# Kernel optimization log

Hardware: AMD Instinct MI355X
Metric: run time of the kernel (lower is better)

## Reference

```python
import jax, jax.numpy as jnp
import numpy as np

N_NODES = 100000
D = 40


def sgconv(x, src, dst, W, b, n_nodes):
    """PyG SGConv with K=1: symmetric gcn_norm with self-loops, then linear."""
    # add self loops
    loop = jnp.arange(n_nodes, dtype=src.dtype)
    s = jnp.concatenate([src, loop])
    d = jnp.concatenate([dst, loop])
    ones = jnp.ones(s.shape[0], dtype=x.dtype)
    deg = jax.ops.segment_sum(ones, d, num_segments=n_nodes)
    dinv = jnp.where(deg > 0, jax.lax.rsqrt(deg), 0.0)
    norm = dinv[s] * dinv[d]                      # [E+N]
    msg = norm[:, None] * x[s]                    # gather + scale, [E+N, D]
    agg = jax.ops.segment_sum(msg, d, num_segments=n_nodes)  # scatter-add, [N, D]
    return agg @ W.T + b


def setup_inputs() -> dict:
    key = jax.random.key(0)
    k1, k2, k3, k4, k5, k6 = jax.random.split(key, 6)
    x = jax.random.normal(k1, (N_NODES, D), dtype=jnp.float32)
    edge_index = jax.random.randint(k2, (2, 1600000), 0, N_NODES, dtype=jnp.int64)
    s = 1.0 / np.sqrt(D)
    W1 = jax.random.uniform(k3, (D, D), jnp.float32, -s, s)
    b1 = jax.random.uniform(k4, (D,), jnp.float32, -s, s)
    W2 = jax.random.uniform(k5, (D, D), jnp.float32, -s, s)
    b2 = jax.random.uniform(k6, (D,), jnp.float32, -s, s)
    return {"x": x, "edge_index": edge_index, "W1": W1, "b1": b1, "W2": W2, "b2": b2}


def reference(x, edge_index, W1, b1, W2, b2):
    src, dst = edge_index[0], edge_index[1]
    n = x.shape[0]
    h = jax.nn.relu(sgconv(x, src, dst, W1, b1, n))
    out = sgconv(h, src, dst, W2, b2, n)
    return out.reshape(n * out.shape[1])  # generalizes x.view(1600)
```

## Files before the change

kernel.cpp:

```cpp
#include <hip/hip_runtime.h>
#include <hip/hip_fp16.h>

#define DD 40
#define PITER 32
#define NP 512
#define SROW_LD 44
#define SWT_LD 41
#define GC_PAD 16

__global__ void k_binA(const int* __restrict__ src, const int* __restrict__ dst,
                       int* __restrict__ gcur, unsigned* __restrict__ ebin,
                       int E, int PS, unsigned M, int CAPB) {
  __shared__ int hist[NP];
  __shared__ int curs[NP];
  const int tid = threadIdx.x;
  hist[tid] = 0;
  hist[tid + 256] = 0;
  __syncthreads();
  const int base = blockIdx.x * (256 * PITER);
  for (int it = 0; it < PITER; ++it) {
    int i = base + it * 256 + tid;
    if (i < E) {
      unsigned t = (unsigned)dst[i];
      int b = (int)(((unsigned long long)t * M) >> 31);
      atomicAdd(&hist[b], 1);
    }
  }
  __syncthreads();
#pragma unroll
  for (int q = 0; q < 2; ++q) {
    int b = tid + q * 256;
    int h = hist[b];
    int old = h ? atomicAdd(&gcur[b * GC_PAD], h) : 0;
    curs[b] = b * CAPB + old;
  }
  __syncthreads();
  for (int it = 0; it < PITER; ++it) {
    int i = base + it * 256 + tid;
    if (i < E) {
      unsigned t = (unsigned)dst[i];
      int b = (int)(((unsigned long long)t * M) >> 31);
      unsigned local = t - (unsigned)(b * PS);
      int pos = atomicAdd(&curs[b], 1);
      ebin[pos] = (local << 17) | (unsigned)src[i];
    }
  }
}

__global__ __launch_bounds__(256) void k_partB(
    const unsigned* __restrict__ ebin, const int* __restrict__ gcur,
    int* __restrict__ ideg, int* __restrict__ cursor, float* __restrict__ dinv,
    int* __restrict__ es, int PS, int CAPB, int CAPE, int n) {
  __shared__ int sdeg[256];
  __shared__ int sbuf[2][256];
  __shared__ int scur[256];
  const int p = blockIdx.x;
  const int tid = threadIdx.x;
  const int start = p * CAPB;
  const int cnt = gcur[p * GC_PAD];

  sdeg[tid] = 0;
  __syncthreads();
  for (int i = tid; i < cnt; i += 256) atomicAdd(&sdeg[ebin[start + i] >> 17], 1);
  __syncthreads();

  int v = sdeg[tid];
  sbuf[0][tid] = v;
  __syncthreads();
  int pi = 0;
  for (int off = 1; off < 256; off <<= 1) {
    int x = sbuf[pi][tid];
    if (tid >= off) x += sbuf[pi][tid - off];
    sbuf[pi ^ 1][tid] = x;
    __syncthreads();
    pi ^= 1;
  }
  int incl = sbuf[pi][tid];
  scur[tid] = incl - v;

  const int node = p * PS + tid;
  if (tid < PS && node < n) {
    ideg[node] = v;
    cursor[node] = p * CAPE + incl;
    dinv[node] = rsqrtf((float)(v + 1));
  }
  __syncthreads();

  for (int i = tid; i < cnt; i += 256) {
    unsigned pk = ebin[start + i];
    int l = (int)(pk >> 17);
    int pos = atomicAdd(&scur[l], 1);
    es[p * CAPE + pos] = (int)(pk & 0x1FFFFu);
  }
}

__global__ void k_prescale(const float4* __restrict__ x4, const float* __restrict__ dinv,
                           uint2* __restrict__ xs8, int n4) {
  int i = blockIdx.x * blockDim.x + threadIdx.x;
  if (i < n4) {
    float w = dinv[i / 10];
    float4 v = x4[i];
    __half2 ha = __float22half2_rn(make_float2(v.x * w, v.y * w));
    __half2 hb = __float22half2_rn(make_float2(v.z * w, v.w * w));
    uint2 u;
    u.x = *(unsigned*)&ha;
    u.y = *(unsigned*)&hb;
    xs8[i] = u;
  }
}

template <int OUT_HALF>
__global__ __launch_bounds__(256) void k_layer(
    const uint4* __restrict__ in4, const int* __restrict__ es,
    const int* __restrict__ ideg, const int* __restrict__ cursor,
    const float* __restrict__ dinv, const float* __restrict__ W,
    const float* __restrict__ bias, float* __restrict__ outf,
    __half2* __restrict__ outh, int n) {
  __shared__ float sWT[DD * SWT_LD];
  __shared__ float sb[DD];
  __shared__ float srow[48][SROW_LD];
  const int tid = threadIdx.x;

  const int w = tid >> 6, lane = tid & 63;
  const int g = lane / 5, pos = lane - g * 5;
  const int v = blockIdx.x * 48 + w * 12 + g;

#define ACC8(U, A)                                   \
  {                                                  \
    const __half2* hh = (const __half2*)&(U);        \
    float2 f0 = __half22float2(hh[0]);               \
    float2 f1 = __half22float2(hh[1]);               \
    float2 f2 = __half22float2(hh[2]);               \
    float2 f3 = __half22float2(hh[3]);               \
    A[0] += f0.x; A[1] += f0.y; A[2] += f1.x;        \
    A[3] += f1.y; A[4] += f2.x; A[5] += f2.y;        \
    A[6] += f3.x; A[7] += f3.y;                      \
  }

  if (g < 12 && v < n) {
    const int e1 = cursor[v];
    int e = e1 - ideg[v];
    float a[8], b[8];
    {
      uint4 u = in4[(size_t)v * 5 + pos];
      const __half2* hh = (const __half2*)&u;
      float2 f0 = __half22float2(hh[0]);
      float2 f1 = __half22float2(hh[1]);
      float2 f2 = __half22float2(hh[2]);
      float2 f3 = __half22float2(hh[3]);
      a[0] = f0.x; a[1] = f0.y; a[2] = f1.x; a[3] = f1.y;
      a[4] = f2.x; a[5] = f2.y; a[6] = f3.x; a[7] = f3.y;
#pragma unroll
      for (int q = 0; q < 8; ++q) b[q] = 0.f;
    }
    int n0, n1, n2, n3, n4, n5, n6, n7;
    bool have = (e + 7 < e1);
    if (have) {
      n0 = es[e];     n1 = es[e + 1]; n2 = es[e + 2]; n3 = es[e + 3];
      n4 = es[e + 4]; n5 = es[e + 5]; n6 = es[e + 6]; n7 = es[e + 7];
    }
    while (have) {
      int s0 = n0, s1 = n1, s2 = n2, s3 = n3, s4 = n4, s5 = n5, s6 = n6, s7 = n7;
      int en = e + 8;
      have = (en + 7 < e1);
      if (have) {
        n0 = es[en];     n1 = es[en + 1]; n2 = es[en + 2]; n3 = es[en + 3];
        n4 = es[en + 4]; n5 = es[en + 5]; n6 = es[en + 6]; n7 = es[en + 7];
      }
      uint4 u0 = in4[(size_t)s0 * 5 + pos];
      uint4 u1 = in4[(size_t)s1 * 5 + pos];
      uint4 u2 = in4[(size_t)s2 * 5 + pos];
      uint4 u3 = in4[(size_t)s3 * 5 + pos];
      uint4 u4 = in4[(size_t)s4 * 5 + pos];
      uint4 u5 = in4[(size_t)s5 * 5 + pos];
      uint4 u6 = in4[(size_t)s6 * 5 + pos];
      uint4 u7 = in4[(size_t)s7 * 5 + pos];
      ACC8(u0, a); ACC8(u1, b); ACC8(u2, a); ACC8(u3, b);
      ACC8(u4, a); ACC8(u5, b); ACC8(u6, a); ACC8(u7, b);
      e = en;
    }
    for (; e + 3 < e1; e += 4) {
      int s0 = es[e], s1 = es[e + 1], s2 = es[e + 2], s3 = es[e + 3];
      uint4 u0 = in4[(size_t)s0 * 5 + pos];
      uint4 u1 = in4[(size_t)s1 * 5 + pos];
      uint4 u2 = in4[(size_t)s2 * 5 + pos];
      uint4 u3 = in4[(size_t)s3 * 5 + pos];
      ACC8(u0, a); ACC8(u1, b); ACC8(u2, a); ACC8(u3, b);
    }
    for (; e < e1; ++e) {
      uint4 uu = in4[(size_t)es[e] * 5 + pos];
      ACC8(uu, a);
    }
    float* r = &srow[w * 12 + g][pos * 8];
#pragma unroll
    for (int q = 0; q < 8; ++q) r[q] = a[q] + b[q];
  }

  for (int t = tid; t < DD * DD; t += 256) sWT[(t % DD) * SWT_LD + t / DD] = W[t];
  if (tid < DD) sb[tid] = bias[tid];
  __syncthreads();

  if (OUT_HALF) {
    for (int i = tid; i < 48 * 20; i += 256) {
      int l = i / 20, jj = i - l * 20;
      int vv = blockIdx.x * 48 + l;
      if (vv < n) {
        float dv = dinv[vv];
        const float* row = srow[l];
        float s0 = 0.f, s1 = 0.f;
#pragma unroll
        for (int k = 0; k < DD; ++k) {
          s0 = fmaf(row[k], sWT[k * SWT_LD + 2 * jj], s0);
          s1 = fmaf(row[k], sWT[k * SWT_LD + 2 * jj + 1], s1);
        }
        s0 = fmaf(s0, dv, sb[2 * jj]);
        s1 = fmaf(s1, dv, sb[2 * jj + 1]);
        s0 = fmaxf(s0, 0.f) * dv;
        s1 = fmaxf(s1, 0.f) * dv;
        outh[(size_t)vv * 20 + jj] = __float22half2_rn(make_float2(s0, s1));
      }
    }
  } else {
    for (int i = tid; i < 48 * DD; i += 256) {
      int l = i / DD, j = i - l * DD;
      int vv = blockIdx.x * 48 + l;
      if (vv < n) {
        float dv = dinv[vv];
        const float* row = srow[l];
        float acc = 0.f;
#pragma unroll
        for (int k = 0; k < DD; ++k) acc = fmaf(row[k], sWT[k * SWT_LD + j], acc);
        outf[(size_t)vv * DD + j] = fmaf(acc, dv, sb[j]);
      }
    }
  }
#undef ACC8
}

extern "C" void kernel_launch(void* const* d_in, const int* in_sizes, int n_in,
                              void* d_out, int out_size, void* d_ws, size_t ws_size,
                              hipStream_t stream) {
  const float* x = (const float*)d_in[0];
  const int* ei = (const int*)d_in[1];
  const float* W1 = (const float*)d_in[2];
  const float* b1 = (const float*)d_in[3];
  const float* W2 = (const float*)d_in[4];
  const float* b2 = (const float*)d_in[5];

  const int n = in_sizes[0] / DD;
  const int E = in_sizes[1] / 2;
  const int* src = ei;
  const int* dst = ei + E;
  const int n4 = n * (DD / 4);
  const int PS = (n + NP - 1) / NP;
  const unsigned M = (unsigned)((((unsigned long long)1 << 31) + PS - 1) / PS);
  const int CAPB = E / NP + 512;
  const int CAPE = CAPB;
  const int NCH = (E + 256 * PITER - 1) / (256 * PITER);

  float* out = (float*)d_out;

  char* w = (char*)d_ws;
  float* dinv = (float*)w;   w += (size_t)n * 4;
  int* ideg = (int*)w;       w += (size_t)n * 4;
  int* cursor = (int*)w;     w += (size_t)n * 4;
  int* gcur = (int*)w;       w += (size_t)NP * GC_PAD * 4;
  char* ebin_hs = w;         w += (size_t)n * DD * 2;
  int* es = (int*)w;         w += (size_t)NP * CAPE * 4;
  uint2* xs8 = (uint2*)w;    w += (size_t)n * DD * 2;

  unsigned* ebin = (unsigned*)ebin_hs;
  uint2* hs8 = (uint2*)ebin_hs;

  hipMemsetAsync(gcur, 0, (size_t)NP * GC_PAD * 4, stream);

  k_binA<<<NCH, 256, 0, stream>>>(src, dst, gcur, ebin, E, PS, M, CAPB);
  k_partB<<<NP, 256, 0, stream>>>(ebin, gcur, ideg, cursor, dinv, es, PS, CAPB, CAPE, n);
  k_prescale<<<(n4 + 255) / 256, 256, 0, stream>>>((const float4*)x, dinv, xs8, n4);

  const int NBK = (n + 47) / 48;
  k_layer<1><<<NBK, 256, 0, stream>>>((const uint4*)xs8, es, ideg, cursor, dinv,
                                      W1, b1, nullptr, (__half2*)hs8, n);
  k_layer<0><<<NBK, 256, 0, stream>>>((const uint4*)hs8, es, ideg, cursor, dinv,
                                      W2, b2, out, nullptr, n);
}
```

Baseline: 153.4 us.

## Split neighbor lists by source half and sort edges locally before binning

k_binA now sorts each chunk's edges by destination bin in shared memory before writing them out. This turns scattered global stores into more contiguous runs. Each edge is also tagged by whether its source lies in the lower or upper half of the node range. k_partB orders each node's neighbor list as low-half sources first, then high-half sources, and records the split point. k_layer gathers the low half, hits a block barrier, then gathers the high half, aiming for better cache locality on the feature gathers. The costs are extra shared memory, lower occupancy in k_binA, a barrier that can stall warps, and an extra per-node array.

```diff
diff --git a/kernel.cpp b/kernel.cpp
--- a/kernel.cpp
+++ b/kernel.cpp
@@ -7,65 +7,37 @@
 #define SROW_LD 44
 #define SWT_LD 41
 #define GC_PAD 16
-
-__global__ void k_binA(const int* __restrict__ src, const int* __restrict__ dst,
-                       int* __restrict__ gcur, unsigned* __restrict__ ebin,
-                       int E, int PS, unsigned M, int CAPB) {
+#define BAE (256 * PITER)
+
+__global__ __launch_bounds__(256) void k_binA(
+    const int* __restrict__ src, const int* __restrict__ dst,
+    int* __restrict__ gcur, unsigned* __restrict__ ebin,
+    int E, int PS, unsigned M, int CAPB, int H) {
+  __shared__ unsigned ssort[BAE];
+  __shared__ int sdest[BAE];
   __shared__ int hist[NP];
+  __shared__ int binstart[NP];
   __shared__ int curs[NP];
+  __shared__ int win[NP];
+  __shared__ int sbuf[2][256];
   const int tid = threadIdx.x;
+  const int base = blockIdx.x * BAE;
+  const int cnt = min(BAE, E - base);
+
   hist[tid] = 0;
   hist[tid + 256] = 0;
   __syncthreads();
-  const int base = blockIdx.x * (256 * PITER);
   for (int it = 0; it < PITER; ++it) {
-    int i = base + it * 256 + tid;
-    if (i < E) {
-      unsigned t = (unsigned)dst[i];
+    int i = it * 256 + tid;
+    if (i < cnt) {
+      unsigned t = (unsigned)dst[base + i];
       int b = (int)(((unsigned long long)t * M) >> 31);
       atomicAdd(&hist[b], 1);
     }
   }
   __syncthreads();
-#pragma unroll
-  for (int q = 0; q < 2; ++q) {
-    int b = tid + q * 256;
-    int h = hist[b];
-    int old = h ? atomicAdd(&gcur[b * GC_PAD], h) : 0;
-    curs[b] = b * CAPB + old;
-  }
-  __syncthreads();
-  for (int it = 0; it < PITER; ++it) {
-    int i = base + it * 256 + tid;
-    if (i < E) {
-      unsigned t = (unsigned)dst[i];
-      int b = (int)(((unsigned long long)t * M) >> 31);
-      unsigned local = t - (unsigned)(b * PS);
-      int pos = atomicAdd(&curs[b], 1);
-      ebin[pos] = (local << 17) | (unsigned)src[i];
-    }
-  }
-}
-
-__global__ __launch_bounds__(256) void k_partB(
-    const unsigned* __restrict__ ebin, const int* __restrict__ gcur,
-    int* __restrict__ ideg, int* __restrict__ cursor, float* __restrict__ dinv,
-    int* __restrict__ es, int PS, int CAPB, int CAPE, int n) {
-  __shared__ int sdeg[256];
-  __shared__ int sbuf[2][256];
-  __shared__ int scur[256];
-  const int p = blockIdx.x;
-  const int tid = threadIdx.x;
-  const int start = p * CAPB;
-  const int cnt = gcur[p * GC_PAD];
-
-  sdeg[tid] = 0;
-  __syncthreads();
-  for (int i = tid; i < cnt; i += 256) atomicAdd(&sdeg[ebin[start + i] >> 17], 1);
-  __syncthreads();
-
-  int v = sdeg[tid];
-  sbuf[0][tid] = v;
+  int h0 = hist[2 * tid], h1 = hist[2 * tid + 1];
+  sbuf[0][tid] = h0 + h1;
   __syncthreads();
   int pi = 0;
   for (int off = 1; off < 256; off <<= 1) {
@@ -75,12 +47,80 @@
     __syncthreads();
     pi ^= 1;
   }
+  int excl = sbuf[pi][tid] - (h0 + h1);
+  binstart[2 * tid] = excl;
+  binstart[2 * tid + 1] = excl + h0;
+  curs[2 * tid] = excl;
+  curs[2 * tid + 1] = excl + h0;
+#pragma unroll
+  for (int q = 0; q < 2; ++q) {
+    int b = 2 * tid + q;
+    int h = hist[b];
+    win[b] = h ? (b * CAPB + atomicAdd(&gcur[b * GC_PAD], h)) : 0;
+  }
+  __syncthreads();
+  for (int it = 0; it < PITER; ++it) {
+    int i = it * 256 + tid;
+    if (i < cnt) {
+      unsigned t = (unsigned)dst[base + i];
+      int b = (int)(((unsigned long long)t * M) >> 31);
+      unsigned local = t - (unsigned)(b * PS);
+      unsigned s = (unsigned)src[base + i];
+      unsigned hf = (s >= (unsigned)H) ? 0x80000000u : 0u;
+      int pos = atomicAdd(&curs[b], 1);
+      ssort[pos] = hf | (local << 17) | s;
+      sdest[pos] = win[b] + (pos - binstart[b]);
+    }
+  }
+  __syncthreads();
+  for (int k = tid; k < cnt; k += 256) ebin[sdest[k]] = ssort[k];
+}
+
+__global__ __launch_bounds__(256) void k_partB(
+    const unsigned* __restrict__ ebin, const int* __restrict__ gcur,
+    int* __restrict__ ideg, int* __restrict__ dlo, int* __restrict__ cursor,
+    float* __restrict__ dinv, int* __restrict__ es,
+    int PS, int CAPB, int CAPE, int n) {
+  __shared__ int slo[256], shi[256];
+  __shared__ int sbuf[2][256];
+  __shared__ int clo[256], chi[256];
+  const int p = blockIdx.x;
+  const int tid = threadIdx.x;
+  const int start = p * CAPB;
+  const int cnt = gcur[p * GC_PAD];
+
+  slo[tid] = 0;
+  shi[tid] = 0;
+  __syncthreads();
+  for (int i = tid; i < cnt; i += 256) {
+    unsigned pk = ebin[start + i];
+    int l = (int)((pk >> 17) & 0xFF);
+    if (pk & 0x80000000u) atomicAdd(&shi[l], 1);
+    else atomicAdd(&slo[l], 1);
+  }
+  __syncthreads();
+
+  int vlo = slo[tid], vhi = shi[tid];
+  int v = vlo + vhi;
+  sbuf[0][tid] = v;
+  __syncthreads();
+  int pi = 0;
+  for (int off = 1; off < 256; off <<= 1) {
+    int x = sbuf[pi][tid];
+    if (tid >= off) x += sbuf[pi][tid - off];
+    sbuf[pi ^ 1][tid] = x;
+    __syncthreads();
+    pi ^= 1;
+  }
   int incl = sbuf[pi][tid];
-  scur[tid] = incl - v;
+  int rstart = incl - v;
+  clo[tid] = rstart;
+  chi[tid] = rstart + vlo;
 
   const int node = p * PS + tid;
   if (tid < PS && node < n) {
     ideg[node] = v;
+    dlo[node] = vlo;
     cursor[node] = p * CAPE + incl;
     dinv[node] = rsqrtf((float)(v + 1));
   }
@@ -88,8 +128,8 @@
 
   for (int i = tid; i < cnt; i += 256) {
     unsigned pk = ebin[start + i];
-    int l = (int)(pk >> 17);
-    int pos = atomicAdd(&scur[l], 1);
+    int l = (int)((pk >> 17) & 0xFF);
+    int pos = (pk & 0x80000000u) ? atomicAdd(&chi[l], 1) : atomicAdd(&clo[l], 1);
     es[p * CAPE + pos] = (int)(pk & 0x1FFFFu);
   }
 }
@@ -112,10 +152,10 @@
 template <int OUT_HALF>
 __global__ __launch_bounds__(256) void k_layer(
     const uint4* __restrict__ in4, const int* __restrict__ es,
-    const int* __restrict__ ideg, const int* __restrict__ cursor,
-    const float* __restrict__ dinv, const float* __restrict__ W,
-    const float* __restrict__ bias, float* __restrict__ outf,
-    __half2* __restrict__ outh, int n) {
+    const int* __restrict__ ideg, const int* __restrict__ dlo,
+    const int* __restrict__ cursor, const float* __restrict__ dinv,
+    const float* __restrict__ W, const float* __restrict__ bias,
+    float* __restrict__ outf, __half2* __restrict__ outh, int n) {
   __shared__ float sWT[DD * SWT_LD];
   __shared__ float sb[DD];
   __shared__ float srow[48][SROW_LD];
@@ -124,6 +164,7 @@
   const int w = tid >> 6, lane = tid & 63;
   const int g = lane / 5, pos = lane - g * 5;
   const int v = blockIdx.x * 48 + w * 12 + g;
+  const bool act = (g < 12 && v < n);
 
 #define ACC8(U, A)                                   \
   {                                                  \
@@ -137,24 +178,27 @@
     A[6] += f3.x; A[7] += f3.y;                      \
   }
 
-  if (g < 12 && v < n) {
-    const int e1 = cursor[v];
-    int e = e1 - ideg[v];
-    float a[8], b[8];
-    {
-      uint4 u = in4[(size_t)v * 5 + pos];
-      const __half2* hh = (const __half2*)&u;
-      float2 f0 = __half22float2(hh[0]);
-      float2 f1 = __half22float2(hh[1]);
-      float2 f2 = __half22float2(hh[2]);
-      float2 f3 = __half22float2(hh[3]);
-      a[0] = f0.x; a[1] = f0.y; a[2] = f1.x; a[3] = f1.y;
-      a[4] = f2.x; a[5] = f2.y; a[6] = f3.x; a[7] = f3.y;
-#pragma unroll
-      for (int q = 0; q < 8; ++q) b[q] = 0.f;
-    }
+  float a[8], b[8];
+  int mid = 0, e1 = 0;
+  if (act) {
+    e1 = cursor[v];
+    int e0 = e1 - ideg[v];
+    mid = e0 + dlo[v];
+    uint4 u = in4[(size_t)v * 5 + pos];
+    const __half2* hh = (const __half2*)&u;
+    float2 f0 = __half22float2(hh[0]);
+    float2 f1 = __half22float2(hh[1]);
+    float2 f2 = __half22float2(hh[2]);
+    float2 f3 = __half22float2(hh[3]);
+    a[0] = f0.x; a[1] = f0.y; a[2] = f1.x; a[3] = f1.y;
+    a[4] = f2.x; a[5] = f2.y; a[6] = f3.x; a[7] = f3.y;
+#pragma unroll
+    for (int q = 0; q < 8; ++q) b[q] = 0.f;
+  }
+
+  auto gather = [&](int e, int eend) {
     int n0, n1, n2, n3, n4, n5, n6, n7;
-    bool have = (e + 7 < e1);
+    bool have = (e + 7 < eend);
     if (have) {
       n0 = es[e];     n1 = es[e + 1]; n2 = es[e + 2]; n3 = es[e + 3];
       n4 = es[e + 4]; n5 = es[e + 5]; n6 = es[e + 6]; n7 = es[e + 7];
@@ -162,7 +206,7 @@
     while (have) {
       int s0 = n0, s1 = n1, s2 = n2, s3 = n3, s4 = n4, s5 = n5, s6 = n6, s7 = n7;
       int en = e + 8;
-      have = (en + 7 < e1);
+      have = (en + 7 < eend);
       if (have) {
         n0 = es[en];     n1 = es[en + 1]; n2 = es[en + 2]; n3 = es[en + 3];
         n4 = es[en + 4]; n5 = es[en + 5]; n6 = es[en + 6]; n7 = es[en + 7];
@@ -179,7 +223,7 @@
       ACC8(u4, a); ACC8(u5, b); ACC8(u6, a); ACC8(u7, b);
       e = en;
     }
-    for (; e + 3 < e1; e += 4) {
+    for (; e + 3 < eend; e += 4) {
       int s0 = es[e], s1 = es[e + 1], s2 = es[e + 2], s3 = es[e + 3];
       uint4 u0 = in4[(size_t)s0 * 5 + pos];
       uint4 u1 = in4[(size_t)s1 * 5 + pos];
@@ -187,10 +231,16 @@
       uint4 u3 = in4[(size_t)s3 * 5 + pos];
       ACC8(u0, a); ACC8(u1, b); ACC8(u2, a); ACC8(u3, b);
     }
-    for (; e < e1; ++e) {
+    for (; e < eend; ++e) {
       uint4 uu = in4[(size_t)es[e] * 5 + pos];
       ACC8(uu, a);
     }
+  };
+
+  if (act) gather(e1 - ideg[v] + 0, mid);
+  __syncthreads();
+  if (act) {
+    gather(mid, e1);
     float* r = &srow[w * 12 + g][pos * 8];
 #pragma unroll
     for (int q = 0; q < 8; ++q) r[q] = a[q] + b[q];
@@ -256,13 +306,15 @@
   const unsigned M = (unsigned)((((unsigned long long)1 << 31) + PS - 1) / PS);
   const int CAPB = E / NP + 512;
   const int CAPE = CAPB;
-  const int NCH = (E + 256 * PITER - 1) / (256 * PITER);
+  const int NCH = (E + BAE - 1) / BAE;
+  const int H = n / 2;
 
   float* out = (float*)d_out;
 
   char* w = (char*)d_ws;
   float* dinv = (float*)w;   w += (size_t)n * 4;
   int* ideg = (int*)w;       w += (size_t)n * 4;
+  int* dloA = (int*)w;       w += (size_t)n * 4;
   int* cursor = (int*)w;     w += (size_t)n * 4;
   int* gcur = (int*)w;       w += (size_t)NP * GC_PAD * 4;
   char* ebin_hs = w;         w += (size_t)n * DD * 2;
@@ -274,13 +326,14 @@
 
   hipMemsetAsync(gcur, 0, (size_t)NP * GC_PAD * 4, stream);
 
-  k_binA<<<NCH, 256, 0, stream>>>(src, dst, gcur, ebin, E, PS, M, CAPB);
-  k_partB<<<NP, 256, 0, stream>>>(ebin, gcur, ideg, cursor, dinv, es, PS, CAPB, CAPE, n);
+  k_binA<<<NCH, 256, 0, stream>>>(src, dst, gcur, ebin, E, PS, M, CAPB, H);
+  k_partB<<<NP, 256, 0, stream>>>(ebin, gcur, ideg, dloA, cursor, dinv, es,
+                                  PS, CAPB, CAPE, n);
   k_prescale<<<(n4 + 255) / 256, 256, 0, stream>>>((const float4*)x, dinv, xs8, n4);
 
   const int NBK = (n + 47) / 48;
-  k_layer<1><<<NBK, 256, 0, stream>>>((const uint4*)xs8, es, ideg, cursor, dinv,
+  k_layer<1><<<NBK, 256, 0, stream>>>((const uint4*)xs8, es, ideg, dloA, cursor, dinv,
                                       W1, b1, nullptr, (__half2*)hs8, n);
-  k_layer<0><<<NBK, 256, 0, stream>>>((const uint4*)hs8, es, ideg, cursor, dinv,
+  k_layer<0><<<NBK, 256, 0, stream>>>((const uint4*)hs8, es, ideg, dloA, cursor, dinv,
                                       W2, b2, out, nullptr, n);
 }
```

After: 155.4 us. No clear change (+1.3%).

## Sort edge bins in LDS before scatter and split node features into aligned arrays

Applied to the files above, without the earlier changes.

The binning kernel now counting-sorts each chunk of edges by bin in shared memory, then writes them out contiguously, so global writes to ebin are coalesced runs instead of scattered atomics-driven stores. Node features (fp16, 80 bytes) are split into a 64-byte main array plus a 16-byte tail array, so the four main gather lanes read from 64-byte-aligned rows with shift addressing rather than a multiply by 5. The cost is extra shared memory in binA (about 64KB), which lowers occupancy, plus an added scan. The partB index gets masked to 8 bits.

```diff
diff --git a/kernel.cpp b/kernel.cpp
--- a/kernel.cpp
+++ b/kernel.cpp
@@ -7,44 +7,71 @@
 #define SROW_LD 44
 #define SWT_LD 41
 #define GC_PAD 16
-
-__global__ void k_binA(const int* __restrict__ src, const int* __restrict__ dst,
-                       int* __restrict__ gcur, unsigned* __restrict__ ebin,
-                       int E, int PS, unsigned M, int CAPB) {
+#define BAE (256 * PITER)
+
+__global__ __launch_bounds__(256) void k_binA(
+    const int* __restrict__ src, const int* __restrict__ dst,
+    int* __restrict__ gcur, unsigned* __restrict__ ebin,
+    int E, int PS, unsigned M, int CAPB) {
+  __shared__ unsigned ssort[BAE];
+  __shared__ int sdest[BAE];
   __shared__ int hist[NP];
+  __shared__ int binstart[NP];
   __shared__ int curs[NP];
+  __shared__ int win[NP];
+  __shared__ int sbuf[2][256];
   const int tid = threadIdx.x;
+  const int base = blockIdx.x * BAE;
+  const int cnt = min(BAE, E - base);
+
   hist[tid] = 0;
   hist[tid + 256] = 0;
   __syncthreads();
-  const int base = blockIdx.x * (256 * PITER);
   for (int it = 0; it < PITER; ++it) {
-    int i = base + it * 256 + tid;
-    if (i < E) {
-      unsigned t = (unsigned)dst[i];
+    int i = it * 256 + tid;
+    if (i < cnt) {
+      unsigned t = (unsigned)dst[base + i];
       int b = (int)(((unsigned long long)t * M) >> 31);
       atomicAdd(&hist[b], 1);
     }
   }
   __syncthreads();
+  int h0 = hist[2 * tid], h1 = hist[2 * tid + 1];
+  sbuf[0][tid] = h0 + h1;
+  __syncthreads();
+  int pi = 0;
+  for (int off = 1; off < 256; off <<= 1) {
+    int x = sbuf[pi][tid];
+    if (tid >= off) x += sbuf[pi][tid - off];
+    sbuf[pi ^ 1][tid] = x;
+    __syncthreads();
+    pi ^= 1;
+  }
+  int excl = sbuf[pi][tid] - (h0 + h1);
+  binstart[2 * tid] = excl;
+  binstart[2 * tid + 1] = excl + h0;
+  curs[2 * tid] = excl;
+  curs[2 * tid + 1] = excl + h0;
 #pragma unroll
   for (int q = 0; q < 2; ++q) {
-    int b = tid + q * 256;
+    int b = 2 * tid + q;
     int h = hist[b];
-    int old = h ? atomicAdd(&gcur[b * GC_PAD], h) : 0;
-    curs[b] = b * CAPB + old;
+    win[b] = h ? (b * CAPB + atomicAdd(&gcur[b * GC_PAD], h)) : 0;
   }
   __syncthreads();
   for (int it = 0; it < PITER; ++it) {
-    int i = base + it * 256 + tid;
-    if (i < E) {
-      unsigned t = (unsigned)dst[i];
+    int i = it * 256 + tid;
+    if (i < cnt) {
+      unsigned t = (unsigned)dst[base + i];
       int b = (int)(((unsigned long long)t * M) >> 31);
       unsigned local = t - (unsigned)(b * PS);
       int pos = atomicAdd(&curs[b], 1);
-      ebin[pos] = (local << 17) | (unsigned)src[i];
-    }
-  }
+      ssort[pos] = (local << 17) | (unsigned)src[base + i];
+      sdest[pos] = win[b] + (pos - binstart[b]);
+    }
+  }
+  __syncthreads();
+  for (int k = tid; k < cnt; k += 256) ebin[sdest[k]] = ssort[k];
 }
 
 __global__ __launch_bounds__(256) void k_partB(
@@ -61,7 +88,8 @@
 
   sdeg[tid] = 0;
   __syncthreads();
-  for (int i = tid; i < cnt; i += 256) atomicAdd(&sdeg[ebin[start + i] >> 17], 1);
+  for (int i = tid; i < cnt; i += 256)
+    atomicAdd(&sdeg[(ebin[start + i] >> 17) & 0xFF], 1);
   __syncthreads();
 
   int v = sdeg[tid];
@@ -88,34 +116,40 @@
 
   for (int i = tid; i < cnt; i += 256) {
     unsigned pk = ebin[start + i];
-    int l = (int)(pk >> 17);
+    int l = (int)((pk >> 17) & 0xFF);
     int pos = atomicAdd(&scur[l], 1);
     es[p * CAPE + pos] = (int)(pk & 0x1FFFFu);
   }
 }
 
 __global__ void k_prescale(const float4* __restrict__ x4, const float* __restrict__ dinv,
-                           uint2* __restrict__ xs8, int n4) {
+                           uint4* __restrict__ xs_m, uint4* __restrict__ xs_t, int n5) {
   int i = blockIdx.x * blockDim.x + threadIdx.x;
-  if (i < n4) {
-    float w = dinv[i / 10];
-    float4 v = x4[i];
-    __half2 ha = __float22half2_rn(make_float2(v.x * w, v.y * w));
-    __half2 hb = __float22half2_rn(make_float2(v.z * w, v.w * w));
-    uint2 u;
-    u.x = *(unsigned*)&ha;
-    u.y = *(unsigned*)&hb;
-    xs8[i] = u;
+  if (i < n5) {
+    int node = i / 5, part = i - node * 5;
+    float w = dinv[node];
+    float4 va = x4[node * 10 + part * 2];
+    float4 vb = x4[node * 10 + part * 2 + 1];
+    __half2 h0 = __float22half2_rn(make_float2(va.x * w, va.y * w));
+    __half2 h1 = __float22half2_rn(make_float2(va.z * w, va.w * w));
+    __half2 h2 = __float22half2_rn(make_float2(vb.x * w, vb.y * w));
+    __half2 h3 = __float22half2_rn(make_float2(vb.z * w, vb.w * w));
+    uint4 u;
+    u.x = *(unsigned*)&h0; u.y = *(unsigned*)&h1;
+    u.z = *(unsigned*)&h2; u.w = *(unsigned*)&h3;
+    if (part < 4) xs_m[(size_t)node * 4 + part] = u;
+    else xs_t[node] = u;
   }
 }
 
 template <int OUT_HALF>
 __global__ __launch_bounds__(256) void k_layer(
-    const uint4* __restrict__ in4, const int* __restrict__ es,
-    const int* __restrict__ ideg, const int* __restrict__ cursor,
-    const float* __restrict__ dinv, const float* __restrict__ W,
-    const float* __restrict__ bias, float* __restrict__ outf,
-    __half2* __restrict__ outh, int n) {
+    const uint4* __restrict__ in_m, const uint4* __restrict__ in_t,
+    const int* __restrict__ es, const int* __restrict__ ideg,
+    const int* __restrict__ cursor, const float* __restrict__ dinv,
+    const float* __restrict__ W, const float* __restrict__ bias,
+    float* __restrict__ outf, __half2* __restrict__ outh_m,
+    __half2* __restrict__ outh_t, int n) {
   __shared__ float sWT[DD * SWT_LD];
   __shared__ float sb[DD];
   __shared__ float srow[48][SROW_LD];
@@ -124,6 +158,9 @@
   const int w = tid >> 6, lane = tid & 63;
   const int g = lane / 5, pos = lane - g * 5;
   const int v = blockIdx.x * 48 + w * 12 + g;
+
+  const uint4* gbase = (pos < 4) ? (in_m + pos) : in_t;
+  const int gshift = (pos < 4) ? 2 : 0;
 
 #define ACC8(U, A)                                   \
   {                                                  \
@@ -136,13 +173,14 @@
     A[3] += f1.y; A[4] += f2.x; A[5] += f2.y;        \
     A[6] += f3.x; A[7] += f3.y;                      \
   }
+#define GLD(S) gbase[(size_t)((S) << gshift)]
 
   if (g < 12 && v < n) {
     const int e1 = cursor[v];
     int e = e1 - ideg[v];
     float a[8], b[8];
     {
-      uint4 u = in4[(size_t)v * 5 + pos];
+      uint4 u = GLD(v);
       const __half2* hh = (const __half2*)&u;
       float2 f0 = __half22float2(hh[0]);
       float2 f1 = __half22float2(hh[1]);
@@ -167,28 +205,28 @@
         n0 = es[en];     n1 = es[en + 1]; n2 = es[en + 2]; n3 = es[en + 3];
         n4 = es[en + 4]; n5 = es[en + 5]; n6 = es[en + 6]; n7 = es[en + 7];
       }
-      uint4 u0 = in4[(size_t)s0 * 5 + pos];
-      uint4 u1 = in4[(size_t)s1 * 5 + pos];
-      uint4 u2 = in4[(size_t)s2 * 5 + pos];
-      uint4 u3 = in4[(size_t)s3 * 5 + pos];
-      uint4 u4 = in4[(size_t)s4 * 5 + pos];
-      uint4 u5 = in4[(size_t)s5 * 5 + pos];
-      uint4 u6 = in4[(size_t)s6 * 5 + pos];
-      uint4 u7 = in4[(size_t)s7 * 5 + pos];
+      uint4 u0 = GLD(s0);
+      uint4 u1 = GLD(s1);
+      uint4 u2 = GLD(s2);
+      uint4 u3 = GLD(s3);
+      uint4 u4 = GLD(s4);
+      uint4 u5 = GLD(s5);
+      uint4 u6 = GLD(s6);
+      uint4 u7 = GLD(s7);
       ACC8(u0, a); ACC8(u1, b); ACC8(u2, a); ACC8(u3, b);
       ACC8(u4, a); ACC8(u5, b); ACC8(u6, a); ACC8(u7, b);
       e = en;
     }
     for (; e + 3 < e1; e += 4) {
       int s0 = es[e], s1 = es[e + 1], s2 = es[e + 2], s3 = es[e + 3];
-      uint4 u0 = in4[(size_t)s0 * 5 + pos];
-      uint4 u1 = in4[(size_t)s1 * 5 + pos];
-      uint4 u2 = in4[(size_t)s2 * 5 + pos];
-      uint4 u3 = in4[(size_t)s3 * 5 + pos];
+      uint4 u0 = GLD(s0);
+      uint4 u1 = GLD(s1);
+      uint4 u2 = GLD(s2);
+      uint4 u3 = GLD(s3);
       ACC8(u0, a); ACC8(u1, b); ACC8(u2, a); ACC8(u3, b);
     }
     for (; e < e1; ++e) {
-      uint4 uu = in4[(size_t)es[e] * 5 + pos];
+      uint4 uu = GLD(es[e]);
       ACC8(uu, a);
     }
     float* r = &srow[w * 12 + g][pos * 8];
@@ -217,7 +255,9 @@
         s1 = fmaf(s1, dv, sb[2 * jj + 1]);
         s0 = fmaxf(s0, 0.f) * dv;
         s1 = fmaxf(s1, 0.f) * dv;
-        outh[(size_t)vv * 20 + jj] = __float22half2_rn(make_float2(s0, s1));
+        __half2 hv = __float22half2_rn(make_float2(s0, s1));
+        if (jj < 16) outh_m[(size_t)vv * 16 + jj] = hv;
+        else outh_t[(size_t)vv * 4 + (jj - 16)] = hv;
       }
     }
   } else {
@@ -234,6 +274,7 @@
       }
     }
   }
+#undef GLD
 #undef ACC8
 }
 
@@ -251,12 +292,11 @@
   const int E = in_sizes[1] / 2;
   const int* src = ei;
   const int* dst = ei + E;
-  const int n4 = n * (DD / 4);
   const int PS = (n + NP - 1) / NP;
   const unsigned M = (unsigned)((((unsigned long long)1 << 31) + PS - 1) / PS);
   const int CAPB = E / NP + 512;
   const int CAPE = CAPB;
-  const int NCH = (E + 256 * PITER - 1) / (256 * PITER);
+  const int NCH = (E + BAE - 1) / BAE;
 
   float* out = (float*)d_out;
 
@@ -265,22 +305,25 @@
   int* ideg = (int*)w;       w += (size_t)n * 4;
   int* cursor = (int*)w;     w += (size_t)n * 4;
   int* gcur = (int*)w;       w += (size_t)NP * GC_PAD * 4;
-  char* ebin_hs = w;         w += (size_t)n * DD * 2;
+  char* ebin_hs = w;         w += (size_t)n * 80;
   int* es = (int*)w;         w += (size_t)NP * CAPE * 4;
-  uint2* xs8 = (uint2*)w;    w += (size_t)n * DD * 2;
+  uint4* xs_m = (uint4*)w;   w += (size_t)n * 64;
+  uint4* xs_t = (uint4*)w;   w += (size_t)n * 16;
 
   unsigned* ebin = (unsigned*)ebin_hs;
-  uint2* hs8 = (uint2*)ebin_hs;
+  uint4* hs_m = (uint4*)ebin_hs;
+  uint4* hs_t = (uint4*)(ebin_hs + (size_t)n * 64);
 
   hipMemsetAsync(gcur, 0, (size_t)NP * GC_PAD * 4, stream);
 
   k_binA<<<NCH, 256, 0, stream>>>(src, dst, gcur, ebin, E, PS, M, CAPB);
   k_partB<<<NP, 256, 0, stream>>>(ebin, gcur, ideg, cursor, dinv, es, PS, CAPB, CAPE, n);
-  k_prescale<<<(n4 + 255) / 256, 256, 0, stream>>>((const float4*)x, dinv, xs8, n4);
+  const int n5 = n * 5;
+  k_prescale<<<(n5 + 255) / 256, 256, 0, stream>>>((const float4*)x, dinv, xs_m, xs_t, n5);
 
   const int NBK = (n + 47) / 48;
-  k_layer<1><<<NBK, 256, 0, stream>>>((const uint4*)xs8, es, ideg, cursor, dinv,
-                                      W1, b1, nullptr, (__half2*)hs8, n);
-  k_layer<0><<<NBK, 256, 0, stream>>>((const uint4*)hs8, es, ideg, cursor, dinv,
-                                      W2, b2, out, nullptr, n);
-}
+  k_layer<1><<<NBK, 256, 0, stream>>>(xs_m, xs_t, es, ideg, cursor, dinv, W1, b1,
+                                      nullptr, (__half2*)hs_m, (__half2*)hs_t, n);
+  k_layer<0><<<NBK, 256, 0, stream>>>(hs_m, hs_t, es, ideg, cursor, dinv, W2, b2,
+                                      out, nullptr, nullptr, n);
+}
```

Result: slower. 160.5 us (+4.6%).
